# Kernel optimization log

Hardware: AMD Instinct MI355X
Metric: run time of the kernel (lower is better)

## Reference

```python
import jax, jax.numpy as jnp
import numpy as np

K = 3
ACCEPTANCE_RADIUS = 0.1
CONFIDENCE_THRESHOLD = 0.05
CORRESPONDENCE_THRESHOLD = 3
NUM_REFINEMENT_STEPS = 5
EPS = 1e-5


def _pair_dist2(ref_pts, src_pts):
    # ref: (..., M, 3), src: (..., N, 3) -> squared distances (..., M, N)
    r2 = jnp.sum(ref_pts * ref_pts, axis=-1)[..., :, None]
    s2 = jnp.sum(src_pts * src_pts, axis=-1)[..., None, :]
    cross = jnp.einsum('...mc,...nc->...mn', ref_pts, src_pts)
    return r2 + s2 - 2.0 * cross


def _svd_rigid(H, cr, cs):
    # H = sum w (src-cs)(ref-cr)^T, torch convention H = U S V^T; R = V E U^T
    U, S, Vh = jnp.linalg.svd(H)
    V = jnp.swapaxes(Vh, -1, -2)
    Ut = jnp.swapaxes(U, -1, -2)
    d = jnp.sign(jnp.linalg.det(V @ Ut))
    V = V.at[..., :, 2].multiply(d[..., None])  # E = diag(1,1,sign(det))
    R = V @ Ut
    t = cr - jnp.einsum('...cd,...d->...c', R, cs)
    return R, t


def _procrustes_batch(w, ref_pts, src_pts):
    # dense weighted Procrustes per patch; w: (B,M,N), ref: (B,M,3), src: (B,N,3)
    wn = w / (jnp.sum(w, axis=(1, 2), keepdims=True) + EPS)
    cr = jnp.einsum('bmn,bmc->bc', wn, ref_pts)
    cs = jnp.einsum('bmn,bnc->bc', wn, src_pts)
    refc = ref_pts - cr[:, None, :]
    srcc = src_pts - cs[:, None, :]
    A = jnp.einsum('bmn,bmd->bnd', wn, refc)
    H = jnp.einsum('bnc,bnd->bcd', srcc, A)  # (B,3,3)
    return _svd_rigid(H, cr, cs)


def _procrustes_global(w, ref_pts, src_pts):
    # single transform over all stacked correspondences (zero weights = absent)
    wn = w / (jnp.sum(w) + EPS)
    cr = jnp.einsum('bmn,bmc->c', wn, ref_pts)
    cs = jnp.einsum('bmn,bnc->c', wn, src_pts)
    refc = ref_pts - cr
    srcc = src_pts - cs
    A = jnp.einsum('bmn,bmd->bnd', wn, refc)
    H = jnp.einsum('bnc,bnd->cd', srcc, A)  # (3,3)
    return _svd_rigid(H, cr, cs)


def setup_inputs() -> dict:
    key = jax.random.key(0)
    kr, ks, kn = jax.random.split(key, 3)
    B, M, N = 128, 64, 64
    ref = jax.random.uniform(kr, (B, M, 3), jnp.float32)
    src = ref + 0.01 * jax.random.normal(ks, (B, N, 3), jnp.float32)
    # scores correlated with proximity so top-k/mutual selection yields real inliers
    d = jnp.sqrt(jnp.maximum(_pair_dist2(ref, src), 0.0))
    score_mat = 2.0 - 10.0 * d + 0.1 * jax.random.normal(kn, (B, M, N), jnp.float32)
    return {"ref_knn_points": ref, "src_knn_points": src, "score_mat": score_mat}


def reference(ref_knn_points, src_knn_points, score_mat):
    B, M, N = score_mat.shape
    exp_scores = jnp.exp(score_mat)

    # --- top-k selection along each dim + confidence threshold (mutual=True) ---
    _, ref_idx = jax.lax.top_k(exp_scores, K)                      # (B,M,K) over src dim
    bi = jnp.arange(B)[:, None, None]
    mi = jnp.arange(M)[None, :, None]
    ref_sel = jnp.zeros((B, M, N), bool).at[bi, mi, ref_idx].set(True)
    _, src_idx = jax.lax.top_k(jnp.swapaxes(exp_scores, 1, 2), K)  # (B,N,K) over ref dim
    ni = jnp.arange(N)[None, :, None]
    src_sel = jnp.swapaxes(jnp.zeros((B, N, M), bool).at[bi, ni, src_idx].set(True), 1, 2)
    conf = exp_scores > CONFIDENCE_THRESHOLD
    corr_mat = ref_sel & src_sel & conf
    w = exp_scores * corr_mat                                       # dense corr scores

    # --- per-patch candidate transforms (weighted Procrustes) ---
    Rb, tb = _procrustes_batch(w, ref_knn_points, src_knn_points)   # (B,3,3),(B,3)

    # --- verify every candidate transform against all correspondences ---
    moved = jnp.einsum('bnc,pdc->pbnd', src_knn_points, Rb) + tb[:, None, None, :]
    d2 = _pair_dist2(ref_knn_points[None], moved)                   # (P,B,M,N)
    r2 = ACCEPTANCE_RADIUS * ACCEPTANCE_RADIUS
    inlier = (d2 < r2) & corr_mat[None]
    counts = jnp.sum(inlier, axis=(1, 2, 3))
    valid = jnp.sum(corr_mat, axis=(1, 2)) >= CORRESPONDENCE_THRESHOLD
    counts = jnp.where(valid, counts, -1)
    best = jnp.argmax(counts)

    # --- iterative global refinement ---
    cur_w = w * inlier[best]
    R, t = _procrustes_global(cur_w, ref_knn_points, src_knn_points)
    for _ in range(NUM_REFINEMENT_STEPS - 1):
        moved = src_knn_points @ R.T + t                            # (B,N,3)
        d2 = _pair_dist2(ref_knn_points, moved)                     # (B,M,N)
        cur_w = w * (d2 < r2)
        R, t = _procrustes_global(cur_w, ref_knn_points, src_knn_points)

    transform = jnp.eye(4, dtype=R.dtype).at[:3, :3].set(R).at[:3, 3].set(t)
    return w, transform
```

## Files before the change

### kernel.cpp

```cpp
#include <hip/hip_runtime.h>
#include <math.h>

#define NB 128
#define NM 64
#define NN 64
#define KSEL 3
#define SLOTS (NM * KSEL)
#define TOTSLOTS (NB * SLOTS)
#define CONF_TH 0.05f
#define RAD2 0.01f
#define EPSV 1e-5

struct Slot {
  float4 s;
  float4 r;
};

struct Ws {
  Slot  pack[TOTSLOTS];
  float Rb[NB * 9];
  float tb[NB * 3];
  int   ncorr[NB];
  int   bestkey;
};

__device__ __forceinline__ void mat3vec(const double H[3][3], const double v[3], double o[3]) {
  o[0] = H[0][0] * v[0] + H[0][1] * v[1] + H[0][2] * v[2];
  o[1] = H[1][0] * v[0] + H[1][1] * v[1] + H[1][2] * v[2];
  o[2] = H[2][0] * v[0] + H[2][1] * v[1] + H[2][2] * v[2];
}

__device__ __forceinline__ void cross3(const double a[3], const double b[3], double o[3]) {
  o[0] = a[1] * b[2] - a[2] * b[1];
  o[1] = a[2] * b[0] - a[0] * b[2];
  o[2] = a[0] * b[1] - a[1] * b[0];
}

__device__ void solve_rigid(const double* acc, float* Rf, float* tf) {
  double denom = acc[0] + EPSV;
  double cr[3], cs[3];
  for (int i = 0; i < 3; i++) { cr[i] = acc[1 + i] / denom; cs[i] = acc[4 + i] / denom; }
  double sig = acc[0] / denom;
  double H[3][3];
  for (int c = 0; c < 3; c++)
    for (int d = 0; d < 3; d++)
      H[c][d] = acc[7 + c * 3 + d] / denom - (2.0 - sig) * cs[c] * cr[d];

  double A[3][3], V[3][3] = {{1,0,0},{0,1,0},{0,0,1}};
  for (int i = 0; i < 3; i++)
    for (int j = 0; j < 3; j++) {
      double s = 0;
      for (int k = 0; k < 3; k++) s += H[k][i] * H[k][j];
      A[i][j] = s;
    }
  for (int sweep = 0; sweep < 15; sweep++) {
    for (int p = 0; p < 3; p++) {
      for (int q = p + 1; q < 3; q++) {
        double apq = A[p][q];
        if (fabs(apq) <= 1e-14 * (fabs(A[p][p]) + fabs(A[q][q]))) continue;
        double tau = (A[q][q] - A[p][p]) / (2.0 * apq);
        double tt = (tau >= 0.0) ? 1.0 / (tau + sqrt(1.0 + tau * tau))
                                 : 1.0 / (tau - sqrt(1.0 + tau * tau));
        double c = 1.0 / sqrt(1.0 + tt * tt), s = tt * c;
        for (int k = 0; k < 3; k++) {
          double akp = A[k][p], akq = A[k][q];
          A[k][p] = c * akp - s * akq;
          A[k][q] = s * akp + c * akq;
        }
        for (int k = 0; k < 3; k++) {
          double apk = A[p][k], aqk = A[q][k];
          A[p][k] = c * apk - s * aqk;
          A[q][k] = s * apk + c * aqk;
        }
        for (int k = 0; k < 3; k++) {
          double vkp = V[k][p], vkq = V[k][q];
          V[k][p] = c * vkp - s * vkq;
          V[k][q] = s * vkp + c * vkq;
        }
      }
    }
  }
  double lam[3] = {A[0][0], A[1][1], A[2][2]};
  int i0 = 0, i1 = 1, i2 = 2, tmp;
  if (lam[i0] < lam[i1]) { tmp = i0; i0 = i1; i1 = tmp; }
  if (lam[i0] < lam[i2]) { tmp = i0; i0 = i2; i2 = tmp; }
  if (lam[i1] < lam[i2]) { tmp = i1; i1 = i2; i2 = tmp; }

  double v1[3] = {V[0][i0], V[1][i0], V[2][i0]};
  double v2[3] = {V[0][i1], V[1][i1], V[2][i1]};
  double u1[3], u2[3];
  mat3vec(H, v1, u1);
  double n1 = sqrt(u1[0]*u1[0] + u1[1]*u1[1] + u1[2]*u1[2]);
  if (n1 > 1e-30) { u1[0] /= n1; u1[1] /= n1; u1[2] /= n1; }
  else { u1[0] = 1; u1[1] = 0; u1[2] = 0; }
  mat3vec(H, v2, u2);
  double d12 = u1[0]*u2[0] + u1[1]*u2[1] + u1[2]*u2[2];
  u2[0] -= d12 * u1[0]; u2[1] -= d12 * u1[1]; u2[2] -= d12 * u1[2];
  double n2 = sqrt(u2[0]*u2[0] + u2[1]*u2[1] + u2[2]*u2[2]);
  if (n2 > 1e-30) { u2[0] /= n2; u2[1] /= n2; u2[2] /= n2; }
  else {
    double ax[3] = { (fabs(u1[0]) < 0.9) ? 1.0 : 0.0, (fabs(u1[0]) < 0.9) ? 0.0 : 1.0, 0.0 };
    cross3(u1, ax, u2);
    double nn = sqrt(u2[0]*u2[0] + u2[1]*u2[1] + u2[2]*u2[2]);
    u2[0] /= nn; u2[1] /= nn; u2[2] /= nn;
  }
  double u3[3], v3[3];
  cross3(u1, u2, u3);
  cross3(v1, v2, v3);
  double Rd[3][3];
  for (int i = 0; i < 3; i++)
    for (int j = 0; j < 3; j++)
      Rd[i][j] = v1[i] * u1[j] + v2[i] * u2[j] + v3[i] * u3[j];
  for (int i = 0; i < 3; i++) {
    double t = cr[i] - (Rd[i][0] * cs[0] + Rd[i][1] * cs[1] + Rd[i][2] * cs[2]);
    tf[i] = (float)t;
    for (int j = 0; j < 3; j++) Rf[i * 3 + j] = (float)Rd[i][j];
  }
}

__global__ __launch_bounds__(256) void kA(const float* __restrict__ ref,
                                          const float* __restrict__ src,
                                          const float* __restrict__ score,
                                          float* __restrict__ wout,
                                          Ws* __restrict__ ws) {
  const int b = blockIdx.x;
  const int tid = threadIdx.x;
  __shared__ float se[NM][NN + 1];
  __shared__ unsigned long long rowmask[NM], colmask[NN];
  __shared__ int rsel[NM][KSEL];
  __shared__ float red[16][SLOTS + 1];
  __shared__ double acc[16];
  __shared__ int scount;

  const float* sc = score + (size_t)b * NM * NN;
  for (int i = tid; i < NM * NN; i += 256)
    se[i >> 6][i & 63] = expf(sc[i]);
  if (tid == 0) scount = 0;
  __syncthreads();

  if (tid < NM) {
    const int m = tid;
    float v0 = -1e30f, v1 = -1e30f, v2 = -1e30f; int j0 = 0, j1 = 0, j2 = 0;
    for (int n = 0; n < NN; n++) {
      float v = se[m][n];
      if (v > v0) { v2 = v1; j2 = j1; v1 = v0; j1 = j0; v0 = v; j0 = n; }
      else if (v > v1) { v2 = v1; j2 = j1; v1 = v; j1 = n; }
      else if (v > v2) { v2 = v; j2 = n; }
    }
    rsel[m][0] = j0; rsel[m][1] = j1; rsel[m][2] = j2;
    rowmask[m] = (1ull << j0) | (1ull << j1) | (1ull << j2);
  } else if (tid < 128) {
    const int n = tid - 64;
    float v0 = -1e30f, v1 = -1e30f, v2 = -1e30f; int j0 = 0, j1 = 0, j2 = 0;
    for (int m = 0; m < NM; m++) {
      float v = se[m][n];
      if (v > v0) { v2 = v1; j2 = j1; v1 = v0; j1 = j0; v0 = v; j0 = m; }
      else if (v > v1) { v2 = v1; j2 = j1; v1 = v; j1 = m; }
      else if (v > v2) { v2 = v; j2 = m; }
    }
    colmask[n] = (1ull << j0) | (1ull << j1) | (1ull << j2);
  }
  __syncthreads();

  float* wo = wout + (size_t)b * NM * NN;
  for (int i = tid; i < NM * NN; i += 256) {
    int m = i >> 6, n = i & 63;
    float e = se[m][n];
    bool corr = ((rowmask[m] >> n) & 1ull) && ((colmask[n] >> m) & 1ull) && (e > CONF_TH);
    wo[i] = corr ? e : 0.0f;
  }

  if (tid < SLOTS) {
    int m = tid / 3;
    int k = tid - m * 3;
    int n = rsel[m][k];
    float e = se[m][n];
    bool corr = ((colmask[n] >> m) & 1ull) && (e > CONF_TH);
    float cw = corr ? e : 0.0f;
    float rx = ref[((size_t)b * NM + m) * 3 + 0];
    float ry = ref[((size_t)b * NM + m) * 3 + 1];
    float rz = ref[((size_t)b * NM + m) * 3 + 2];
    float sx = src[((size_t)b * NN + n) * 3 + 0];
    float sy = src[((size_t)b * NN + n) * 3 + 1];
    float sz = src[((size_t)b * NN + n) * 3 + 2];
    ws->pack[b * SLOTS + tid].s = make_float4(sx, sy, sz, cw);
    ws->pack[b * SLOTS + tid].r = make_float4(rx, ry, rz, 0.0f);
    if (corr) atomicAdd(&scount, 1);
    red[0][tid] = cw;
    red[1][tid] = cw * rx;  red[2][tid] = cw * ry;  red[3][tid] = cw * rz;
    red[4][tid] = cw * sx;  red[5][tid] = cw * sy;  red[6][tid] = cw * sz;
    red[7][tid]  = cw * sx * rx; red[8][tid]  = cw * sx * ry; red[9][tid]  = cw * sx * rz;
    red[10][tid] = cw * sy * rx; red[11][tid] = cw * sy * ry; red[12][tid] = cw * sy * rz;
    red[13][tid] = cw * sz * rx; red[14][tid] = cw * sz * ry; red[15][tid] = cw * sz * rz;
  }
  __syncthreads();
  if (tid < 16) {
    double s = 0;
    for (int i = 0; i < SLOTS; i++) s += (double)red[tid][i];
    acc[tid] = s;
  }
  __syncthreads();
  if (tid == 0) {
    float Rf[9], tf[3];
    solve_rigid(acc, Rf, tf);
    for (int i = 0; i < 9; i++) ws->Rb[b * 9 + i] = Rf[i];
    for (int i = 0; i < 3; i++) ws->tb[b * 3 + i] = tf[i];
    ws->ncorr[b] = scount;
    if (b == 0) ws->bestkey = 0;
  }
}

__global__ __launch_bounds__(256) void kB(Ws* __restrict__ ws) {
  const int p = blockIdx.x;
  const int tid = threadIdx.x;
  float R[9], T[3];
#pragma unroll
  for (int i = 0; i < 9; i++) R[i] = ws->Rb[p * 9 + i];
#pragma unroll
  for (int i = 0; i < 3; i++) T[i] = ws->tb[p * 3 + i];

  int cnt = 0;
  for (int g = tid; g < TOTSLOTS; g += 256) {
    float4 S = ws->pack[g].s;
    float4 Rv = ws->pack[g].r;
    float sx = S.x, sy = S.y, sz = S.z;
    float rx = Rv.x, ry = Rv.y, rz = Rv.z;
    float mx = R[0] * sx + R[1] * sy + R[2] * sz + T[0];
    float my = R[3] * sx + R[4] * sy + R[5] * sz + T[1];
    float mz = R[6] * sx + R[7] * sy + R[8] * sz + T[2];
    float d2 = (rx * rx + ry * ry + rz * rz) + (mx * mx + my * my + mz * mz)
             - 2.0f * (rx * mx + ry * my + rz * mz);
    cnt += (S.w > 0.0f && d2 < RAD2) ? 1 : 0;
  }
  __shared__ int sred[256];
  sred[tid] = cnt;
  __syncthreads();
  for (int s = 128; s > 0; s >>= 1) {
    if (tid < s) sred[tid] += sred[tid + s];
    __syncthreads();
  }
  if (tid == 0) {
    int c = (ws->ncorr[p] >= 3) ? sred[0] : -1;
    int key = ((c + 1) << 8) | (127 - p);
    atomicMax(&ws->bestkey, key);
  }
}

__global__ __launch_bounds__(1024) void kC(float* __restrict__ outT,
                                           Ws* __restrict__ ws) {
  const int tid = threadIdx.x;
  const int wid = tid >> 6, lane = tid & 63;
  __shared__ float sR[9], sT[3];
  __shared__ double wsum[16][16];
  __shared__ double acc[16];
  if (tid == 0) {
    int p = 127 - (ws->bestkey & 0xFF);
    for (int i = 0; i < 9; i++) sR[i] = ws->Rb[p * 9 + i];
    for (int i = 0; i < 3; i++) sT[i] = ws->tb[p * 3 + i];
  }
  __syncthreads();

  for (int iter = 0; iter < 5; iter++) {
    float R0 = sR[0], R1 = sR[1], R2 = sR[2];
    float R3 = sR[3], R4 = sR[4], R5 = sR[5];
    float R6 = sR[6], R7 = sR[7], R8 = sR[8];
    float T0 = sT[0], T1 = sT[1], T2 = sT[2];
    float la[16];
#pragma unroll
    for (int q = 0; q < 16; q++) la[q] = 0.0f;

#pragma unroll 4
    for (int g = tid; g < TOTSLOTS; g += 1024) {
      float4 S = ws->pack[g].s;
      float4 Rv = ws->pack[g].r;
      float sx = S.x, sy = S.y, sz = S.z;
      float rx = Rv.x, ry = Rv.y, rz = Rv.z;
      float mx = R0 * sx + R1 * sy + R2 * sz + T0;
      float my = R3 * sx + R4 * sy + R5 * sz + T1;
      float mz = R6 * sx + R7 * sy + R8 * sz + T2;
      float d2 = (rx * rx + ry * ry + rz * rz) + (mx * mx + my * my + mz * mz)
               - 2.0f * (rx * mx + ry * my + rz * mz);
      float w_ = (d2 < RAD2) ? S.w : 0.0f;
      float wsx = w_ * sx, wsy = w_ * sy, wsz = w_ * sz;
      la[0]  += w_;
      la[1]  += w_ * rx;  la[2]  += w_ * ry;  la[3]  += w_ * rz;
      la[4]  += wsx;      la[5]  += wsy;      la[6]  += wsz;
      la[7]  += wsx * rx; la[8]  += wsx * ry; la[9]  += wsx * rz;
      la[10] += wsy * rx; la[11] += wsy * ry; la[12] += wsy * rz;
      la[13] += wsz * rx; la[14] += wsz * ry; la[15] += wsz * rz;
    }
#pragma unroll
    for (int q = 0; q < 16; q++) {
      float v = la[q];
      for (int off = 32; off > 0; off >>= 1) v += __shfl_down(v, off);
      if (lane == 0) wsum[q][wid] = (double)v;
    }
    __syncthreads();
    if (tid < 16) {
      double s = 0;
      for (int k = 0; k < 16; k++) s += wsum[tid][k];
      acc[tid] = s;
    }
    __syncthreads();
    if (tid == 0) {
      float Rf[9], tf[3];
      solve_rigid(acc, Rf, tf);
      for (int i = 0; i < 9; i++) sR[i] = Rf[i];
      for (int i = 0; i < 3; i++) sT[i] = tf[i];
    }
    __syncthreads();
  }

  if (tid == 0) {
    outT[0] = sR[0]; outT[1] = sR[1]; outT[2]  = sR[2]; outT[3]  = sT[0];
    outT[4] = sR[3]; outT[5] = sR[4]; outT[6]  = sR[5]; outT[7]  = sT[1];
    outT[8] = sR[6]; outT[9] = sR[7]; outT[10] = sR[8]; outT[11] = sT[2];
    outT[12] = 0.0f; outT[13] = 0.0f; outT[14] = 0.0f; outT[15] = 1.0f;
  }
}

extern "C" void kernel_launch(void* const* d_in, const int* in_sizes, int n_in,
                              void* d_out, int out_size, void* d_ws, size_t ws_size,
                              hipStream_t stream) {
  const float* ref   = (const float*)d_in[0];
  const float* src   = (const float*)d_in[1];
  const float* score = (const float*)d_in[2];
  float* w    = (float*)d_out;
  float* outT = (float*)d_out + (size_t)NB * NM * NN;
  Ws* ws = (Ws*)d_ws;

  kA<<<NB, 256, 0, stream>>>(ref, src, score, w, ws);
  kB<<<NB, 256, 0, stream>>>(ws);
  kC<<<1, 1024, 0, stream>>>(outT, ws);
}
```

Before: 203.4 us.

## Spread refinement kernel across 48 blocks with software grid barrier

New measurement: 199.9 us. About the same (-1.7%).

```diff
diff --git a/kernel.cpp b/kernel.cpp
--- a/kernel.cpp
+++ b/kernel.cpp
@@ -10,6 +10,8 @@
 #define CONF_TH 0.05f
 #define RAD2 0.01f
 #define EPSV 1e-5
+#define CBLK 48
+#define CTHR 512
 
 struct Slot {
   float4 s;
@@ -17,11 +19,15 @@
 };
 
 struct Ws {
-  Slot  pack[TOTSLOTS];
-  float Rb[NB * 9];
-  float tb[NB * 3];
-  int   ncorr[NB];
-  int   bestkey;
+  Slot   pack[TOTSLOTS];
+  float  Rb[NB * 9];
+  float  tb[NB * 3];
+  int    ncorr[NB];
+  int    bestkey;
+  int    bar_cnt;
+  int    bar_gen;
+  double partial[CBLK][16];
+  float  cur[12];
 };
 
 __device__ __forceinline__ void mat3vec(const double H[3][3], const double v[3], double o[3]) {
@@ -118,6 +124,24 @@
   }
 }
 
+__device__ __forceinline__ void gbar(int* cnt, int* gen) {
+  __syncthreads();
+  if (threadIdx.x == 0) {
+    int g = __hip_atomic_load(gen, __ATOMIC_RELAXED, __HIP_MEMORY_SCOPE_AGENT);
+    __threadfence();
+    int old = __hip_atomic_fetch_add(cnt, 1, __ATOMIC_ACQ_REL, __HIP_MEMORY_SCOPE_AGENT);
+    if (old == CBLK - 1) {
+      __hip_atomic_store(cnt, 0, __ATOMIC_RELAXED, __HIP_MEMORY_SCOPE_AGENT);
+      __threadfence();
+      __hip_atomic_fetch_add(gen, 1, __ATOMIC_ACQ_REL, __HIP_MEMORY_SCOPE_AGENT);
+    } else {
+      while (__hip_atomic_load(gen, __ATOMIC_ACQUIRE, __HIP_MEMORY_SCOPE_AGENT) == g)
+        __builtin_amdgcn_s_sleep(1);
+    }
+  }
+  __syncthreads();
+}
+
 __global__ __launch_bounds__(256) void kA(const float* __restrict__ ref,
                                           const float* __restrict__ src,
                                           const float* __restrict__ score,
@@ -206,7 +230,7 @@
     for (int i = 0; i < 9; i++) ws->Rb[b * 9 + i] = Rf[i];
     for (int i = 0; i < 3; i++) ws->tb[b * 3 + i] = tf[i];
     ws->ncorr[b] = scount;
-    if (b == 0) ws->bestkey = 0;
+    if (b == 0) { ws->bestkey = 0; ws->bar_cnt = 0; ws->bar_gen = 0; }
   }
 }
 
@@ -246,75 +270,95 @@
   }
 }
 
-__global__ __launch_bounds__(1024) void kC(float* __restrict__ outT,
+__global__ __launch_bounds__(CTHR) void kC(float* __restrict__ outT,
                                            Ws* __restrict__ ws) {
-  const int tid = threadIdx.x;
-  const int wid = tid >> 6, lane = tid & 63;
-  __shared__ float sR[9], sT[3];
-  __shared__ double wsum[16][16];
-  __shared__ double acc[16];
-  if (tid == 0) {
-    int p = 127 - (ws->bestkey & 0xFF);
-    for (int i = 0; i < 9; i++) sR[i] = ws->Rb[p * 9 + i];
-    for (int i = 0; i < 3; i++) sT[i] = ws->tb[p * 3 + i];
-  }
-  __syncthreads();
+  const int tid = threadIdx.x, bid = blockIdx.x;
+  const int lane = tid & 63, wid = tid >> 6;
+  __shared__ double lred[16][CTHR / 64];
+  __shared__ double accs[16];
+  __shared__ float sRt[12];
+
+  const int g = bid * CTHR + tid;
+  const float4 S  = ws->pack[g].s;
+  const float4 Rv = ws->pack[g].r;
+  const float sx = S.x, sy = S.y, sz = S.z, w0 = S.w;
+  const float rx = Rv.x, ry = Rv.y, rz = Rv.z;
+  const float rr = rx * rx + ry * ry + rz * rz;
 
   for (int iter = 0; iter < 5; iter++) {
-    float R0 = sR[0], R1 = sR[1], R2 = sR[2];
-    float R3 = sR[3], R4 = sR[4], R5 = sR[5];
-    float R6 = sR[6], R7 = sR[7], R8 = sR[8];
-    float T0 = sT[0], T1 = sT[1], T2 = sT[2];
+    float Rm[12];
+    if (iter == 0) {
+      int p = 127 - (ws->bestkey & 0xFF);
+#pragma unroll
+      for (int i = 0; i < 9; i++) Rm[i] = ws->Rb[p * 9 + i];
+#pragma unroll
+      for (int i = 0; i < 3; i++) Rm[9 + i] = ws->tb[p * 3 + i];
+    } else {
+#pragma unroll
+      for (int i = 0; i < 12; i++)
+        Rm[i] = __hip_atomic_load(&ws->cur[i], __ATOMIC_RELAXED, __HIP_MEMORY_SCOPE_AGENT);
+    }
+
+    float mx = Rm[0] * sx + Rm[1] * sy + Rm[2] * sz + Rm[9];
+    float my = Rm[3] * sx + Rm[4] * sy + Rm[5] * sz + Rm[10];
+    float mz = Rm[6] * sx + Rm[7] * sy + Rm[8] * sz + Rm[11];
+    float d2 = rr + (mx * mx + my * my + mz * mz)
+             - 2.0f * (rx * mx + ry * my + rz * mz);
+    float w_ = (d2 < RAD2) ? w0 : 0.0f;
+    float wsx = w_ * sx, wsy = w_ * sy, wsz = w_ * sz;
     float la[16];
-#pragma unroll
-    for (int q = 0; q < 16; q++) la[q] = 0.0f;
-
-#pragma unroll 4
-    for (int g = tid; g < TOTSLOTS; g += 1024) {
-      float4 S = ws->pack[g].s;
-      float4 Rv = ws->pack[g].r;
-      float sx = S.x, sy = S.y, sz = S.z;
-      float rx = Rv.x, ry = Rv.y, rz = Rv.z;
-      float mx = R0 * sx + R1 * sy + R2 * sz + T0;
-      float my = R3 * sx + R4 * sy + R5 * sz + T1;
-      float mz = R6 * sx + R7 * sy + R8 * sz + T2;
-      float d2 = (rx * rx + ry * ry + rz * rz) + (mx * mx + my * my + mz * mz)
-               - 2.0f * (rx * mx + ry * my + rz * mz);
-      float w_ = (d2 < RAD2) ? S.w : 0.0f;
-      float wsx = w_ * sx, wsy = w_ * sy, wsz = w_ * sz;
-      la[0]  += w_;
-      la[1]  += w_ * rx;  la[2]  += w_ * ry;  la[3]  += w_ * rz;
-      la[4]  += wsx;      la[5]  += wsy;      la[6]  += wsz;
-      la[7]  += wsx * rx; la[8]  += wsx * ry; la[9]  += wsx * rz;
-      la[10] += wsy * rx; la[11] += wsy * ry; la[12] += wsy * rz;
-      la[13] += wsz * rx; la[14] += wsz * ry; la[15] += wsz * rz;
-    }
+    la[0] = w_;
+    la[1] = w_ * rx;  la[2] = w_ * ry;  la[3] = w_ * rz;
+    la[4] = wsx;      la[5] = wsy;      la[6] = wsz;
+    la[7]  = wsx * rx; la[8]  = wsx * ry; la[9]  = wsx * rz;
+    la[10] = wsy * rx; la[11] = wsy * ry; la[12] = wsy * rz;
+    la[13] = wsz * rx; la[14] = wsz * ry; la[15] = wsz * rz;
+
 #pragma unroll
     for (int q = 0; q < 16; q++) {
       float v = la[q];
       for (int off = 32; off > 0; off >>= 1) v += __shfl_down(v, off);
-      if (lane == 0) wsum[q][wid] = (double)v;
+      if (lane == 0) lred[q][wid] = (double)v;
     }
     __syncthreads();
     if (tid < 16) {
       double s = 0;
-      for (int k = 0; k < 16; k++) s += wsum[tid][k];
-      acc[tid] = s;
-    }
-    __syncthreads();
-    if (tid == 0) {
-      float Rf[9], tf[3];
-      solve_rigid(acc, Rf, tf);
-      for (int i = 0; i < 9; i++) sR[i] = Rf[i];
-      for (int i = 0; i < 3; i++) sT[i] = tf[i];
-    }
-    __syncthreads();
-  }
-
-  if (tid == 0) {
-    outT[0] = sR[0]; outT[1] = sR[1]; outT[2]  = sR[2]; outT[3]  = sT[0];
-    outT[4] = sR[3]; outT[5] = sR[4]; outT[6]  = sR[5]; outT[7]  = sT[1];
-    outT[8] = sR[6]; outT[9] = sR[7]; outT[10] = sR[8]; outT[11] = sT[2];
+#pragma unroll
+      for (int k = 0; k < CTHR / 64; k++) s += lred[tid][k];
+      __hip_atomic_store(&ws->partial[bid][tid], s, __ATOMIC_RELAXED, __HIP_MEMORY_SCOPE_AGENT);
+    }
+    gbar(&ws->bar_cnt, &ws->bar_gen);
+
+    if (bid == 0) {
+      if (tid < 16) {
+        double s = 0;
+        for (int k = 0; k < CBLK; k++)
+          s += __hip_atomic_load(&ws->partial[k][tid], __ATOMIC_RELAXED, __HIP_MEMORY_SCOPE_AGENT);
+        accs[tid] = s;
+      }
+      __syncthreads();
+      if (tid == 0) {
+        float Rf[9], tf[3];
+        solve_rigid(accs, Rf, tf);
+#pragma unroll
+        for (int i = 0; i < 9; i++) sRt[i] = Rf[i];
+#pragma unroll
+        for (int i = 0; i < 3; i++) sRt[9 + i] = tf[i];
+        if (iter < 4) {
+#pragma unroll
+          for (int i = 0; i < 12; i++)
+            __hip_atomic_store(&ws->cur[i], sRt[i], __ATOMIC_RELAXED, __HIP_MEMORY_SCOPE_AGENT);
+        }
+      }
+      __syncthreads();
+    }
+    if (iter < 4) gbar(&ws->bar_cnt, &ws->bar_gen);
+  }
+
+  if (bid == 0 && tid == 0) {
+    outT[0] = sRt[0]; outT[1] = sRt[1]; outT[2]  = sRt[2]; outT[3]  = sRt[9];
+    outT[4] = sRt[3]; outT[5] = sRt[4]; outT[6]  = sRt[5]; outT[7]  = sRt[10];
+    outT[8] = sRt[6]; outT[9] = sRt[7]; outT[10] = sRt[8]; outT[11] = sRt[11];
     outT[12] = 0.0f; outT[13] = 0.0f; outT[14] = 0.0f; outT[15] = 1.0f;
   }
 }
@@ -331,5 +375,5 @@
 
   kA<<<NB, 256, 0, stream>>>(ref, src, score, w, ws);
   kB<<<NB, 256, 0, stream>>>(ws);
-  kC<<<1, 1024, 0, stream>>>(outT, ws);
-}
+  kC<<<CBLK, CTHR, 0, stream>>>(outT, ws);
+}
```
